# Performance work log

Hardware: AMD Instinct MI355X
Metric: run time of the kernel (lower is better)

## Reference

```python
import jax, jax.numpy as jnp
import numpy as np

KL_ALPHA = 0.3
MSE_WEIGHT = 1.0


def setup_inputs() -> dict:
    key = jax.random.key(0)
    ks = jax.random.split(key, 8)
    B, S, V = 4, 512, 32000
    logits = jax.random.normal(ks[0], (B, S + 1, V), dtype=jnp.float32)
    ref_logits = jax.random.normal(ks[1], (B, S + 1, V), dtype=jnp.float32)
    input_ids = jax.random.randint(ks[2], (B, S), 0, V, dtype=jnp.int32)
    attention_mask = jnp.ones((B, S), dtype=jnp.int32)
    word_ids = jnp.sort(jax.random.randint(ks[3], (B, S), 0, S, dtype=jnp.int32), axis=1)
    word_lengths = jax.random.randint(ks[4], (B, S), 0, 12, dtype=jnp.int32)
    log_unigram_frequencies = jax.random.normal(ks[5], (B, S), dtype=jnp.float32)
    labels = jax.random.normal(ks[6], (B, S), dtype=jnp.float32)
    W_head = jax.random.normal(ks[7], (3,), dtype=jnp.float32) * 0.1
    b_head = jnp.zeros((1,), dtype=jnp.float32)
    return dict(logits=logits, ref_logits=ref_logits, input_ids=input_ids,
                attention_mask=attention_mask, word_ids=word_ids,
                word_lengths=word_lengths,
                log_unigram_frequencies=log_unigram_frequencies,
                labels=labels, W_head=W_head, b_head=b_head)


def reference(logits, ref_logits, input_ids, attention_mask, word_ids,
              word_lengths, log_unigram_frequencies, labels, W_head, b_head):
    B, S = input_ids.shape
    lp = jax.nn.log_softmax(logits, axis=-1)                       # [B,S+1,V]
    rlp = jax.lax.stop_gradient(jax.nn.log_softmax(ref_logits, axis=-1))

    # token surprisal = -log p(token_t | prefix): gather from shifted log-probs
    lp_shift = lp[:, :-1, :]                                       # [B,S,V]
    surprisal = -jnp.take_along_axis(lp_shift, input_ids[..., None], axis=2)[..., 0]

    # scatter_add token surprisal into word bins (masked tokens -> bin 0 with value 0)
    mask = word_ids != -1                                          # [B,S]
    masked_surp = surprisal * mask
    masked_wid = jnp.where(mask, word_ids, 0)
    rows = jnp.arange(B)[:, None]
    summed_surprisal = jnp.zeros((B, S), surprisal.dtype).at[rows, masked_wid].add(masked_surp)

    # vectorized per-token gather of word-level features (replaces the Python loop)
    valid = (word_ids >= 0) & (word_ids < S)
    safe = jnp.clip(word_ids, 0, S - 1)
    lens = jnp.take_along_axis(word_lengths, safe, axis=1)
    valid = valid & (lens != -1)
    exp_len = jnp.where(valid, lens.astype(jnp.float32), 0.0)
    exp_freq = jnp.where(valid, jnp.take_along_axis(log_unigram_frequencies, safe, axis=1), 0.0)

    # Linear(3,1) head on [surprisal, length, frequency]
    preds = summed_surprisal * W_head[0] + exp_len * W_head[1] + exp_freq * W_head[2] + b_head[0]

    # masked MSE over valid words (torch boolean extraction == masked mean)
    mask_words = (labels != -1.0).astype(jnp.float32)
    mse_loss = jnp.sum((labels - preds) ** 2 * mask_words) / jnp.sum(mask_words)
    loss = MSE_WEIGHT * mse_loss

    # KL divergence to frozen reference over masked tokens (log_target form)
    kl_mask = jnp.concatenate([jnp.zeros((B, 1), bool), mask[:, :-1]], axis=1).astype(jnp.float32)
    lp_s, rlp_s = lp[:, :-1, :], rlp[:, :-1, :]                    # [B,S,V]
    kl_tok = jnp.sum(jnp.exp(rlp_s) * (rlp_s - lp_s), axis=-1)     # [B,S]
    kl_loss = jnp.sum(kl_tok * kl_mask) / jnp.sum(kl_mask)

    # average log-prob of next tokens and delta vs reference
    shift_ids = input_ids[:, 1:]                                   # [B,S-1]
    ans_mask = attention_mask[:, 1:].astype(jnp.float32)
    g = jnp.take_along_axis(lp[:, :S - 1, :], shift_ids[..., None], axis=2)[..., 0]
    gr = jnp.take_along_axis(rlp[:, :S - 1, :], shift_ids[..., None], axis=2)[..., 0]
    avg_log_prob = jnp.sum(g * ans_mask) / jnp.sum(ans_mask)
    delta_log_prob = avg_log_prob - jnp.sum(gr * ans_mask) / jnp.sum(ans_mask)

    loss = loss + KL_ALPHA * kl_loss
    return loss, preds, mse_loss, kl_loss, avg_log_prob, delta_log_prob
```

## Files before the change

kernel.cpp:

```cpp
#include <hip/hip_runtime.h>
#include <math.h>

#define NB 4
#define NS 512
#define NV 32000
#define NROWS (NB * NS)
#define KL_ALPHA 0.3f
#define SAFE_MAX 60.0f

__global__ __launch_bounds__(256) void krow(const float* __restrict__ logits,
                                            const float* __restrict__ ref_logits,
                                            const int* __restrict__ input_ids,
                                            float* __restrict__ logZx,
                                            float* __restrict__ logZy,
                                            float* __restrict__ klrow,
                                            float* __restrict__ surp,
                                            float* __restrict__ gval,
                                            float* __restrict__ grval) {
    const int row = blockIdx.x;
    const int b = row / NS, s = row - b * NS;
    const size_t base = (size_t)(b * (NS + 1) + s) * NV;
    const float4* __restrict__ x4 = (const float4*)(logits + base);
    const float4* __restrict__ y4 = (const float4*)(ref_logits + base);
    const int tid = threadIdx.x;

    float sx[4] = {0.f, 0.f, 0.f, 0.f};
    float sy[4] = {0.f, 0.f, 0.f, 0.f};
    float ty[4] = {0.f, 0.f, 0.f, 0.f};
    float mx = -INFINITY, my = -INFINITY;

    for (int i = tid; i < NV / 4; i += 256) {
        float4 xv = x4[i];
        float4 yv = y4[i];
        float xs[4] = {xv.x, xv.y, xv.z, xv.w};
        float ys[4] = {yv.x, yv.y, yv.z, yv.w};
#pragma unroll
        for (int j = 0; j < 4; ++j) {
            float xe = xs[j], ye = ys[j];
            mx = fmaxf(mx, xe);
            my = fmaxf(my, ye);
            float ex = __expf(xe);
            float ey = __expf(ye);
            sx[j] += ex;
            sy[j] += ey;
            ty[j] = fmaf(ey, ye - xe, ty[j]);
        }
    }
    float Sx = (sx[0] + sx[1]) + (sx[2] + sx[3]);
    float Sy = (sy[0] + sy[1]) + (sy[2] + sy[3]);
    float Ty = (ty[0] + ty[1]) + (ty[2] + ty[3]);

    for (int off = 32; off > 0; off >>= 1) {
        Sx += __shfl_xor(Sx, off);
        Sy += __shfl_xor(Sy, off);
        Ty += __shfl_xor(Ty, off);
        mx = fmaxf(mx, __shfl_xor(mx, off));
        my = fmaxf(my, __shfl_xor(my, off));
    }
    __shared__ float red[4][5];
    const int wave = tid >> 6, lane = tid & 63;
    if (lane == 0) {
        red[wave][0] = Sx; red[wave][1] = Sy; red[wave][2] = Ty;
        red[wave][3] = mx; red[wave][4] = my;
    }
    __syncthreads();
    float tSx = 0.f, tSy = 0.f, tTy = 0.f, tMx = -INFINITY, tMy = -INFINITY;
#pragma unroll
    for (int w = 0; w < 4; ++w) {
        tSx += red[w][0];
        tSy += red[w][1];
        tTy += red[w][2];
        tMx = fmaxf(tMx, red[w][3]);
        tMy = fmaxf(tMy, red[w][4]);
    }

    float lzx, lzy, klv;
    if (tMx < SAFE_MAX && tMy < SAFE_MAX) {
        lzx = __logf(tSx);
        lzy = __logf(tSy);
        klv = tTy / tSy + lzx - lzy;
    } else {
        float fsx = 0.f, fsy = 0.f, fty = 0.f;
        for (int i = tid; i < NV / 4; i += 256) {
            float4 xv = x4[i];
            float4 yv = y4[i];
            float xs[4] = {xv.x, xv.y, xv.z, xv.w};
            float ys[4] = {yv.x, yv.y, yv.z, yv.w};
#pragma unroll
            for (int j = 0; j < 4; ++j) {
                float xe = xs[j], ye = ys[j];
                fsx += __expf(xe - tMx);
                float ey = __expf(ye - tMy);
                fsy += ey;
                fty = fmaf(ey, ye - xe, fty);
            }
        }
        for (int off = 32; off > 0; off >>= 1) {
            fsx += __shfl_xor(fsx, off);
            fsy += __shfl_xor(fsy, off);
            fty += __shfl_xor(fty, off);
        }
        __syncthreads();
        if (lane == 0) { red[wave][0] = fsx; red[wave][1] = fsy; red[wave][2] = fty; }
        __syncthreads();
        float gSx = 0.f, gSy = 0.f, gTy = 0.f;
#pragma unroll
        for (int w = 0; w < 4; ++w) { gSx += red[w][0]; gSy += red[w][1]; gTy += red[w][2]; }
        lzx = tMx + __logf(gSx);
        lzy = tMy + __logf(gSy);
        klv = gTy / gSy + lzx - lzy;
    }

    if (tid == 0) {
        logZx[row] = lzx;
        logZy[row] = lzy;
        klrow[row] = klv;
        int id0 = input_ids[b * NS + s];
        surp[row] = lzx - logits[base + id0];
        if (s < NS - 1) {
            int id1 = input_ids[b * NS + s + 1];
            gval[row]  = logits[base + id1] - lzx;
            grval[row] = ref_logits[base + id1] - lzy;
        } else {
            gval[row] = 0.f;
            grval[row] = 0.f;
        }
    }
}

__global__ __launch_bounds__(1024) void kfinal(const int* __restrict__ input_ids,
                                               const int* __restrict__ attention_mask,
                                               const int* __restrict__ word_ids,
                                               const int* __restrict__ word_lengths,
                                               const float* __restrict__ lufreq,
                                               const float* __restrict__ labels,
                                               const float* __restrict__ W_head,
                                               const float* __restrict__ b_head,
                                               const float* __restrict__ logZx,
                                               const float* __restrict__ logZy,
                                               const float* __restrict__ klrow,
                                               const float* __restrict__ surp,
                                               const float* __restrict__ gval,
                                               const float* __restrict__ grval,
                                               float* __restrict__ out) {
    __shared__ float summed[NROWS];
    const int tid = threadIdx.x;
    for (int p = tid; p < NROWS; p += 1024) summed[p] = 0.f;
    __syncthreads();
    for (int p = tid; p < NROWS; p += 1024) {
        int b = p / NS;
        int wid = word_ids[p];
        if (wid >= 0 && wid < NS) atomicAdd(&summed[b * NS + wid], surp[p]);
    }
    __syncthreads();

    const float W0 = W_head[0], W1 = W_head[1], W2 = W_head[2], bh = b_head[0];
    float mse_n = 0.f, mse_d = 0.f, kl_n = 0.f, kl_d = 0.f;
    float g_n = 0.f, gr_n = 0.f, g_d = 0.f;
    for (int p = tid; p < NROWS; p += 1024) {
        int b = p / NS, s = p - b * NS;
        int wid = word_ids[p];
        bool valid = (wid >= 0) && (wid < NS);
        int safe = wid < 0 ? 0 : (wid > NS - 1 ? NS - 1 : wid);
        int lens = word_lengths[b * NS + safe];
        valid = valid && (lens != -1);
        float el = valid ? (float)lens : 0.f;
        float ef = valid ? lufreq[b * NS + safe] : 0.f;
        float pred = summed[p] * W0 + el * W1 + ef * W2 + bh;
        out[1 + p] = pred;
        float lab = labels[p];
        float mw = (lab != -1.0f) ? 1.f : 0.f;
        float diff = lab - pred;
        mse_n += diff * diff * mw;
        mse_d += mw;
        float km = (s == 0) ? 0.f : ((word_ids[p - 1] != -1) ? 1.f : 0.f);
        kl_n += klrow[p] * km;
        kl_d += km;
        if (s < NS - 1) {
            float am = (float)attention_mask[b * NS + s + 1];
            g_n += gval[p] * am;
            gr_n += grval[p] * am;
            g_d += am;
        }
    }
    for (int off = 32; off > 0; off >>= 1) {
        mse_n += __shfl_xor(mse_n, off);
        mse_d += __shfl_xor(mse_d, off);
        kl_n  += __shfl_xor(kl_n, off);
        kl_d  += __shfl_xor(kl_d, off);
        g_n   += __shfl_xor(g_n, off);
        gr_n  += __shfl_xor(gr_n, off);
        g_d   += __shfl_xor(g_d, off);
    }
    __shared__ float r2[16][7];
    const int wave = tid >> 6, lane = tid & 63;
    if (lane == 0) {
        r2[wave][0] = mse_n; r2[wave][1] = mse_d;
        r2[wave][2] = kl_n;  r2[wave][3] = kl_d;
        r2[wave][4] = g_n;   r2[wave][5] = gr_n; r2[wave][6] = g_d;
    }
    __syncthreads();
    if (tid == 0) {
        float a0 = 0, a1 = 0, a2 = 0, a3 = 0, a4 = 0, a5 = 0, a6 = 0;
        for (int w = 0; w < 16; ++w) {
            a0 += r2[w][0]; a1 += r2[w][1]; a2 += r2[w][2]; a3 += r2[w][3];
            a4 += r2[w][4]; a5 += r2[w][5]; a6 += r2[w][6];
        }
        float mse = a0 / a1;
        float kl = a2 / a3;
        float loss = mse + KL_ALPHA * kl;
        float avg = a4 / a6;
        float delta = avg - a5 / a6;
        out[0] = loss;
        out[1 + NROWS] = mse;
        out[2 + NROWS] = kl;
        out[3 + NROWS] = avg;
        out[4 + NROWS] = delta;
    }
}

extern "C" void kernel_launch(void* const* d_in, const int* in_sizes, int n_in,
                              void* d_out, int out_size, void* d_ws, size_t ws_size,
                              hipStream_t stream) {
    const float* logits        = (const float*)d_in[0];
    const float* ref_logits    = (const float*)d_in[1];
    const int*   input_ids     = (const int*)d_in[2];
    const int*   attention_mask= (const int*)d_in[3];
    const int*   word_ids      = (const int*)d_in[4];
    const int*   word_lengths  = (const int*)d_in[5];
    const float* lufreq        = (const float*)d_in[6];
    const float* labels        = (const float*)d_in[7];
    const float* W_head        = (const float*)d_in[8];
    const float* b_head        = (const float*)d_in[9];
    float* out = (float*)d_out;
    float* ws = (float*)d_ws;

    float* logZx = ws;
    float* logZy = ws + NROWS;
    float* klrow = ws + 2 * NROWS;
    float* surp  = ws + 3 * NROWS;
    float* gvals = ws + 4 * NROWS;
    float* grvals= ws + 5 * NROWS;

    hipLaunchKernelGGL(krow, dim3(NROWS), dim3(256), 0, stream,
                       logits, ref_logits, input_ids,
                       logZx, logZy, klrow, surp, gvals, grvals);
    hipLaunchKernelGGL(kfinal, dim3(1), dim3(1024), 0, stream,
                       input_ids, attention_mask, word_ids, word_lengths,
                       lufreq, labels, W_head, b_head,
                       logZx, logZy, klrow, surp, gvals, grvals, out);
}
```

Measured before the change: 110.0 us.

## Fuse final reduction into row kernel via last-block atomic counter, drop max tracking

Merges the single-block final reduction kernel into the per-row kernel: each block bumps an atomic counter and the last block to finish does the word-bin scatter and loss reductions. This removes a second kernel launch and its dependency gap, at the cost of a memset launch per call. The hot loop no longer tracks running maxima; the max-based recompute now runs only when the sums overflow, underflow or turn NaN. Loads use nontemporal hints so the streamed logits do not displace cache. The risks are overflow detection depending on float inf checks rather than a max threshold, and the last-block reduction running on only 256 threads.

```diff
diff --git a/kernel.cpp b/kernel.cpp
--- a/kernel.cpp
+++ b/kernel.cpp
@@ -6,39 +6,47 @@
 #define NV 32000
 #define NROWS (NB * NS)
 #define KL_ALPHA 0.3f
-#define SAFE_MAX 60.0f
-
-__global__ __launch_bounds__(256) void krow(const float* __restrict__ logits,
-                                            const float* __restrict__ ref_logits,
-                                            const int* __restrict__ input_ids,
-                                            float* __restrict__ logZx,
-                                            float* __restrict__ logZy,
-                                            float* __restrict__ klrow,
-                                            float* __restrict__ surp,
-                                            float* __restrict__ gval,
-                                            float* __restrict__ grval) {
+
+typedef float floatx4 __attribute__((ext_vector_type(4)));
+
+#define WS_KL    0
+#define WS_SURP  (NROWS)
+#define WS_G     (2 * NROWS)
+#define WS_GR    (3 * NROWS)
+#define WS_LZX   (4 * NROWS)
+#define WS_LZY   (5 * NROWS)
+#define WS_CNT   (6 * NROWS)
+
+__global__ __launch_bounds__(256) void krow_fused(
+        const float* __restrict__ logits,
+        const float* __restrict__ ref_logits,
+        const int* __restrict__ input_ids,
+        const int* __restrict__ attention_mask,
+        const int* __restrict__ word_ids,
+        const int* __restrict__ word_lengths,
+        const float* __restrict__ lufreq,
+        const float* __restrict__ labels,
+        const float* __restrict__ W_head,
+        const float* __restrict__ b_head,
+        float* __restrict__ ws,
+        float* __restrict__ out) {
     const int row = blockIdx.x;
     const int b = row / NS, s = row - b * NS;
     const size_t base = (size_t)(b * (NS + 1) + s) * NV;
-    const float4* __restrict__ x4 = (const float4*)(logits + base);
-    const float4* __restrict__ y4 = (const float4*)(ref_logits + base);
+    const floatx4* __restrict__ x4 = (const floatx4*)(logits + base);
+    const floatx4* __restrict__ y4 = (const floatx4*)(ref_logits + base);
     const int tid = threadIdx.x;
 
     float sx[4] = {0.f, 0.f, 0.f, 0.f};
     float sy[4] = {0.f, 0.f, 0.f, 0.f};
     float ty[4] = {0.f, 0.f, 0.f, 0.f};
-    float mx = -INFINITY, my = -INFINITY;
 
     for (int i = tid; i < NV / 4; i += 256) {
-        float4 xv = x4[i];
-        float4 yv = y4[i];
-        float xs[4] = {xv.x, xv.y, xv.z, xv.w};
-        float ys[4] = {yv.x, yv.y, yv.z, yv.w};
+        floatx4 xv = __builtin_nontemporal_load(&x4[i]);
+        floatx4 yv = __builtin_nontemporal_load(&y4[i]);
 #pragma unroll
         for (int j = 0; j < 4; ++j) {
-            float xe = xs[j], ye = ys[j];
-            mx = fmaxf(mx, xe);
-            my = fmaxf(my, ye);
+            float xe = xv[j], ye = yv[j];
             float ex = __expf(xe);
             float ey = __expf(ye);
             sx[j] += ex;
@@ -54,41 +62,51 @@
         Sx += __shfl_xor(Sx, off);
         Sy += __shfl_xor(Sy, off);
         Ty += __shfl_xor(Ty, off);
-        mx = fmaxf(mx, __shfl_xor(mx, off));
-        my = fmaxf(my, __shfl_xor(my, off));
-    }
-    __shared__ float red[4][5];
+    }
+    __shared__ float red[4][3];
     const int wave = tid >> 6, lane = tid & 63;
-    if (lane == 0) {
-        red[wave][0] = Sx; red[wave][1] = Sy; red[wave][2] = Ty;
-        red[wave][3] = mx; red[wave][4] = my;
-    }
-    __syncthreads();
-    float tSx = 0.f, tSy = 0.f, tTy = 0.f, tMx = -INFINITY, tMy = -INFINITY;
-#pragma unroll
-    for (int w = 0; w < 4; ++w) {
-        tSx += red[w][0];
-        tSy += red[w][1];
-        tTy += red[w][2];
-        tMx = fmaxf(tMx, red[w][3]);
-        tMy = fmaxf(tMy, red[w][4]);
-    }
+    if (lane == 0) { red[wave][0] = Sx; red[wave][1] = Sy; red[wave][2] = Ty; }
+    __syncthreads();
+    float tSx = 0.f, tSy = 0.f, tTy = 0.f;
+#pragma unroll
+    for (int w = 0; w < 4; ++w) { tSx += red[w][0]; tSy += red[w][1]; tTy += red[w][2]; }
+
+    bool bad = !(tSx > 1e-35f) || !(tSy > 1e-35f) ||
+               isinf(tSx) || isinf(tSy) || isinf(tTy) || isnan(tTy);
 
     float lzx, lzy, klv;
-    if (tMx < SAFE_MAX && tMy < SAFE_MAX) {
+    if (!bad) {
         lzx = __logf(tSx);
         lzy = __logf(tSy);
         klv = tTy / tSy + lzx - lzy;
     } else {
+        float mx = -INFINITY, my = -INFINITY;
+        for (int i = tid; i < NV / 4; i += 256) {
+            floatx4 xv = x4[i];
+            floatx4 yv = y4[i];
+            mx = fmaxf(mx, fmaxf(fmaxf(xv[0], xv[1]), fmaxf(xv[2], xv[3])));
+            my = fmaxf(my, fmaxf(fmaxf(yv[0], yv[1]), fmaxf(yv[2], yv[3])));
+        }
+        for (int off = 32; off > 0; off >>= 1) {
+            mx = fmaxf(mx, __shfl_xor(mx, off));
+            my = fmaxf(my, __shfl_xor(my, off));
+        }
+        __syncthreads();
+        if (lane == 0) { red[wave][0] = mx; red[wave][1] = my; }
+        __syncthreads();
+        float tMx = -INFINITY, tMy = -INFINITY;
+#pragma unroll
+        for (int w = 0; w < 4; ++w) {
+            tMx = fmaxf(tMx, red[w][0]);
+            tMy = fmaxf(tMy, red[w][1]);
+        }
         float fsx = 0.f, fsy = 0.f, fty = 0.f;
         for (int i = tid; i < NV / 4; i += 256) {
-            float4 xv = x4[i];
-            float4 yv = y4[i];
-            float xs[4] = {xv.x, xv.y, xv.z, xv.w};
-            float ys[4] = {yv.x, yv.y, yv.z, yv.w};
+            floatx4 xv = x4[i];
+            floatx4 yv = y4[i];
 #pragma unroll
             for (int j = 0; j < 4; ++j) {
-                float xe = xs[j], ye = ys[j];
+                float xe = xv[j], ye = yv[j];
                 fsx += __expf(xe - tMx);
                 float ey = __expf(ye - tMy);
                 fsy += ey;
@@ -112,60 +130,53 @@
     }
 
     if (tid == 0) {
-        logZx[row] = lzx;
-        logZy[row] = lzy;
-        klrow[row] = klv;
+        ws[WS_LZX + row] = lzx;
+        ws[WS_LZY + row] = lzy;
+        ws[WS_KL + row] = klv;
         int id0 = input_ids[b * NS + s];
-        surp[row] = lzx - logits[base + id0];
+        ws[WS_SURP + row] = lzx - logits[base + id0];
         if (s < NS - 1) {
             int id1 = input_ids[b * NS + s + 1];
-            gval[row]  = logits[base + id1] - lzx;
-            grval[row] = ref_logits[base + id1] - lzy;
+            ws[WS_G + row]  = logits[base + id1] - lzx;
+            ws[WS_GR + row] = ref_logits[base + id1] - lzy;
         } else {
-            gval[row] = 0.f;
-            grval[row] = 0.f;
-        }
-    }
-}
-
-__global__ __launch_bounds__(1024) void kfinal(const int* __restrict__ input_ids,
-                                               const int* __restrict__ attention_mask,
-                                               const int* __restrict__ word_ids,
-                                               const int* __restrict__ word_lengths,
-                                               const float* __restrict__ lufreq,
-                                               const float* __restrict__ labels,
-                                               const float* __restrict__ W_head,
-                                               const float* __restrict__ b_head,
-                                               const float* __restrict__ logZx,
-                                               const float* __restrict__ logZy,
-                                               const float* __restrict__ klrow,
-                                               const float* __restrict__ surp,
-                                               const float* __restrict__ gval,
-                                               const float* __restrict__ grval,
-                                               float* __restrict__ out) {
+            ws[WS_G + row] = 0.f;
+            ws[WS_GR + row] = 0.f;
+        }
+    }
+
+    __shared__ int is_last;
+    if (tid == 0) {
+        __threadfence();
+        int old = atomicAdd((int*)(ws + WS_CNT), 1);
+        is_last = (old == NROWS - 1) ? 1 : 0;
+    }
+    __syncthreads();
+    if (!is_last) return;
+    __threadfence();
+
     __shared__ float summed[NROWS];
-    const int tid = threadIdx.x;
-    for (int p = tid; p < NROWS; p += 1024) summed[p] = 0.f;
-    __syncthreads();
-    for (int p = tid; p < NROWS; p += 1024) {
-        int b = p / NS;
+    for (int p = tid; p < NROWS; p += 256) summed[p] = 0.f;
+    __syncthreads();
+    for (int p = tid; p < NROWS; p += 256) {
+        int bb = p / NS;
         int wid = word_ids[p];
-        if (wid >= 0 && wid < NS) atomicAdd(&summed[b * NS + wid], surp[p]);
+        if (wid >= 0 && wid < NS) atomicAdd(&summed[bb * NS + wid], ws[WS_SURP + p]);
     }
     __syncthreads();
 
     const float W0 = W_head[0], W1 = W_head[1], W2 = W_head[2], bh = b_head[0];
     float mse_n = 0.f, mse_d = 0.f, kl_n = 0.f, kl_d = 0.f;
     float g_n = 0.f, gr_n = 0.f, g_d = 0.f;
-    for (int p = tid; p < NROWS; p += 1024) {
-        int b = p / NS, s = p - b * NS;
+    for (int p = tid; p < NROWS; p += 256) {
+        int bb = p / NS, ss = p - bb * NS;
         int wid = word_ids[p];
         bool valid = (wid >= 0) && (wid < NS);
         int safe = wid < 0 ? 0 : (wid > NS - 1 ? NS - 1 : wid);
-        int lens = word_lengths[b * NS + safe];
+        int lens = word_lengths[bb * NS + safe];
         valid = valid && (lens != -1);
         float el = valid ? (float)lens : 0.f;
-        float ef = valid ? lufreq[b * NS + safe] : 0.f;
+        float ef = valid ? lufreq[bb * NS + safe] : 0.f;
         float pred = summed[p] * W0 + el * W1 + ef * W2 + bh;
         out[1 + p] = pred;
         float lab = labels[p];
@@ -173,13 +184,13 @@
         float diff = lab - pred;
         mse_n += diff * diff * mw;
         mse_d += mw;
-        float km = (s == 0) ? 0.f : ((word_ids[p - 1] != -1) ? 1.f : 0.f);
-        kl_n += klrow[p] * km;
+        float km = (ss == 0) ? 0.f : ((word_ids[p - 1] != -1) ? 1.f : 0.f);
+        kl_n += ws[WS_KL + p] * km;
         kl_d += km;
-        if (s < NS - 1) {
-            float am = (float)attention_mask[b * NS + s + 1];
-            g_n += gval[p] * am;
-            gr_n += grval[p] * am;
+        if (ss < NS - 1) {
+            float am = (float)attention_mask[bb * NS + ss + 1];
+            g_n += ws[WS_G + p] * am;
+            gr_n += ws[WS_GR + p] * am;
             g_d += am;
         }
     }
@@ -192,8 +203,7 @@
         gr_n  += __shfl_xor(gr_n, off);
         g_d   += __shfl_xor(g_d, off);
     }
-    __shared__ float r2[16][7];
-    const int wave = tid >> 6, lane = tid & 63;
+    __shared__ float r2[4][7];
     if (lane == 0) {
         r2[wave][0] = mse_n; r2[wave][1] = mse_d;
         r2[wave][2] = kl_n;  r2[wave][3] = kl_d;
@@ -202,20 +212,17 @@
     __syncthreads();
     if (tid == 0) {
         float a0 = 0, a1 = 0, a2 = 0, a3 = 0, a4 = 0, a5 = 0, a6 = 0;
-        for (int w = 0; w < 16; ++w) {
+        for (int w = 0; w < 4; ++w) {
             a0 += r2[w][0]; a1 += r2[w][1]; a2 += r2[w][2]; a3 += r2[w][3];
             a4 += r2[w][4]; a5 += r2[w][5]; a6 += r2[w][6];
         }
         float mse = a0 / a1;
         float kl = a2 / a3;
-        float loss = mse + KL_ALPHA * kl;
-        float avg = a4 / a6;
-        float delta = avg - a5 / a6;
-        out[0] = loss;
+        out[0] = mse + KL_ALPHA * kl;
         out[1 + NROWS] = mse;
         out[2 + NROWS] = kl;
-        out[3 + NROWS] = avg;
-        out[4 + NROWS] = delta;
+        out[3 + NROWS] = a4 / a6;
+        out[4 + NROWS] = a4 / a6 - a5 / a6;
     }
 }
 
@@ -235,18 +242,10 @@
     float* out = (float*)d_out;
     float* ws = (float*)d_ws;
 
-    float* logZx = ws;
-    float* logZy = ws + NROWS;
-    float* klrow = ws + 2 * NROWS;
-    float* surp  = ws + 3 * NROWS;
-    float* gvals = ws + 4 * NROWS;
-    float* grvals= ws + 5 * NROWS;
-
-    hipLaunchKernelGGL(krow, dim3(NROWS), dim3(256), 0, stream,
-                       logits, ref_logits, input_ids,
-                       logZx, logZy, klrow, surp, gvals, grvals);
-    hipLaunchKernelGGL(kfinal, dim3(1), dim3(1024), 0, stream,
-                       input_ids, attention_mask, word_ids, word_lengths,
-                       lufreq, labels, W_head, b_head,
-                       logZx, logZy, klrow, surp, gvals, grvals, out);
+    (void)hipMemsetAsync(ws + WS_CNT, 0, sizeof(int), stream);
+
+    hipLaunchKernelGGL(krow_fused, dim3(NROWS), dim3(256), 0, stream,
+                       logits, ref_logits, input_ids, attention_mask,
+                       word_ids, word_lengths, lufreq, labels,
+                       W_head, b_head, ws, out);
 }
```

Result: slower. 193.3 us (+75.8%).
